# Performance work log

Measured on AMD Instinct MI355X. Metric: run time of the kernel, lower is better.

The kernel has to match this reference:

```python
import jax, jax.numpy as jnp
import numpy as np

N = 100000   # nodes
E = 1000000  # edges (before self-loops)
D = 64       # input_dim
H = 64       # hidden_dim
OUT = 8      # output_dim
G = 128      # num graphs in batch


def setup_inputs() -> dict:
    key = jax.random.key(0)
    ks = jax.random.split(key, 8)
    x = jax.random.normal(ks[0], (N, D), jnp.float32)
    edge_index = jax.random.randint(ks[1], (2, E), 0, N)
    edge_attr = jax.random.uniform(ks[2], (E,), jnp.float32)
    batch = jnp.sort(jax.random.randint(ks[3], (N,), 0, G))
    W1 = jax.random.normal(ks[4], (H, D), jnp.float32) / np.float32(np.sqrt(D))
    b1 = jnp.zeros((H,), jnp.float32)
    W2 = jax.random.normal(ks[5], (OUT, H), jnp.float32) / np.float32(np.sqrt(H))
    b2 = jnp.zeros((OUT,), jnp.float32)
    Wopt = jax.random.normal(ks[6], (1, H), jnp.float32) / np.float32(np.sqrt(H))
    bopt = jnp.zeros((1,), jnp.float32)
    return dict(x=x, edge_index=edge_index, edge_attr=edge_attr, batch=batch,
                W1=W1, b1=b1, W2=W2, b2=b2, Wopt=Wopt, bopt=bopt,
                num_graphs=G)


def gcn_conv(x, edge_index, edge_attr, W, b):
    n = x.shape[0]
    loop = jnp.arange(n)
    # add_self_loops with fill_value=1.0
    row = jnp.concatenate([edge_index[0], loop])
    col = jnp.concatenate([edge_index[1], loop])
    ea = jnp.concatenate([edge_attr, jnp.ones((n,), x.dtype)])
    # degree over row (source); >=1 because of self-loops
    deg = jax.ops.segment_sum(jnp.ones(row.shape, x.dtype), row, num_segments=n)
    dis = deg ** -0.5
    norm = dis[row] * dis[col]
    # message: edge_attr * x_j * norm, gathered from source row
    msg = (ea * norm)[:, None] * x[row]          # [E+N, D]
    aggr = jax.ops.segment_sum(msg, col, num_segments=n)  # scatter-add at target
    return aggr @ W.T + b                        # update: linear


def reference(x, edge_index, edge_attr, batch, W1, b1, W2, b2, Wopt, bopt, num_graphs):
    h = jnp.tanh(gcn_conv(x, edge_index, edge_attr, W1, b1))
    out = jax.nn.sigmoid(h @ W2.T + b2)          # [N, OUT]
    counts = jax.ops.segment_sum(jnp.ones((h.shape[0],), h.dtype), batch,
                                 num_segments=num_graphs)
    gemb = jax.ops.segment_sum(h, batch, num_segments=num_graphs)
    gemb = gemb / jnp.maximum(counts, 1.0)[:, None]  # global_mean_pool
    optimal = jax.nn.sigmoid(gemb @ Wopt.T + bopt)   # [G, 1]
    return (out, optimal)
```

## Files before the change

### kernel.cpp

```cpp
#include <hip/hip_runtime.h>
#include <math.h>
#include <stdint.h>

#define DD 64
#define HH 64
#define OUTD 8
#define NG 128
#define PSPLIT 8
#define NB 512
#define CAPD 3072
#define BIN_CHUNK 4096

typedef short short8 __attribute__((ext_vector_type(8)));
typedef float f32x4 __attribute__((ext_vector_type(4)));

__device__ __forceinline__ float sigmoidf_(float v) { return 1.0f / (1.0f + __expf(-v)); }
__device__ __forceinline__ unsigned short f2bf(float f) {
    unsigned u = __float_as_uint(f);
    unsigned r = u + 0x7FFFu + ((u >> 16) & 1u);
    return (unsigned short)(r >> 16);
}
__device__ __forceinline__ float bf2f(unsigned short b) {
    return __uint_as_float(((unsigned)b) << 16);
}
__device__ __forceinline__ float bflo(unsigned q) { return __uint_as_float(q << 16); }
__device__ __forceinline__ float bfhi(unsigned q) { return __uint_as_float(q & 0xFFFF0000u); }

__global__ void init_kernel(int* gcur, int* scur, float* gemb,
                            const int* __restrict__ batch, int* __restrict__ starts, int N) {
    int t = threadIdx.x;
    for (int i = t; i < NB; i += 256) { gcur[i] = 0; scur[i] = 0; }
    for (int i = t; i < NG * HH; i += 256) gemb[i] = 0.0f;
    if (t <= NG) {
        int g = t, lo = 0, hi = N;
        while (lo < hi) {
            int mid = (lo + hi) >> 1;
            if (batch[mid] < g) lo = mid + 1; else hi = mid;
        }
        starts[g] = lo;
    }
}

__global__ __launch_bounds__(256)
void bin_xcvt_kernel(const int* __restrict__ ei, const float* __restrict__ ea,
                     int* gcur, int* scur, int2* __restrict__ dreg,
                     unsigned char* __restrict__ sreg, int E, int range, int nbin,
                     const float4* __restrict__ x4, uint4* __restrict__ xbf, int n8) {
    if (blockIdx.x >= nbin) {
        int i = (blockIdx.x - nbin) * 256 + threadIdx.x;
        if (i < n8) {
            float4 a = x4[i * 2], b = x4[i * 2 + 1];
            uint4 o;
            o.x = (unsigned)f2bf(a.x) | ((unsigned)f2bf(a.y) << 16);
            o.y = (unsigned)f2bf(a.z) | ((unsigned)f2bf(a.w) << 16);
            o.z = (unsigned)f2bf(b.x) | ((unsigned)f2bf(b.y) << 16);
            o.w = (unsigned)f2bf(b.z) | ((unsigned)f2bf(b.w) << 16);
            xbf[i] = o;
        }
        return;
    }
    __shared__ int dcnt[NB], scnt[NB], dbase[NB], sbase[NB];
    int t = threadIdx.x;
    for (int j = t; j < NB; j += 256) { dcnt[j] = 0; scnt[j] = 0; }
    __syncthreads();
    int e0 = blockIdx.x * BIN_CHUNK;
    int lim = min(BIN_CHUNK, E - e0);
    for (int i = t; i < lim; i += 256) {
        int e = e0 + i;
        atomicAdd(&dcnt[ei[E + e] / range], 1);
        atomicAdd(&scnt[ei[e] / range], 1);
    }
    __syncthreads();
    for (int j = t; j < NB; j += 256) {
        int dc = dcnt[j], sc = scnt[j];
        dbase[j] = dc ? atomicAdd(&gcur[j], dc) : 0;
        sbase[j] = sc ? atomicAdd(&scur[j], sc) : 0;
        dcnt[j] = 0; scnt[j] = 0;
    }
    __syncthreads();
    for (int i = t; i < lim; i += 256) {
        int e = e0 + i;
        int c = ei[E + e];
        int r = ei[e];
        int b = c / range, cl = c - b * range;
        int pos = dbase[b] + atomicAdd(&dcnt[b], 1);
        if (pos < CAPD)
            dreg[(size_t)b * CAPD + pos] = make_int2(r | (cl << 20), __float_as_int(ea[e]));
        int sb = r / range;
        int sp = sbase[sb] + atomicAdd(&scnt[sb], 1);
        if (sp < CAPD)
            sreg[(size_t)sb * CAPD + sp] = (unsigned char)(r - sb * range);
    }
}

__global__ __launch_bounds__(256)
void deg_kernel(const unsigned char* __restrict__ sreg, const int* __restrict__ scur,
                float* __restrict__ dis, int N, int range) {
    __shared__ int cnt[257];
    int t = threadIdx.x, b = blockIdx.x;
    for (int j = t; j <= range; j += 256) cnt[j] = 0;
    __syncthreads();
    int n = min(scur[b], CAPD);
    const unsigned char* p = sreg + (size_t)b * CAPD;
    for (int i = t; i < n; i += 256) atomicAdd(&cnt[p[i]], 1);
    __syncthreads();
    for (int j = t; j < range; j += 256) {
        int node = b * range + j;
        if (node < N) dis[node] = rsqrtf(1.0f + (float)cnt[j]);
    }
}

__global__ __launch_bounds__(256)
void csr_kernel(int2* __restrict__ dreg, const int* __restrict__ gcur,
                const float* __restrict__ dis,
                int* __restrict__ colstart, int* __restrict__ colcnt,
                int N, int range) {
    __shared__ int2 recs[CAPD];
    __shared__ int cnt[257], offs_s[257], sc[256];
    int t = threadIdx.x, b = blockIdx.x;
    int n = min(gcur[b], CAPD);
    size_t base = (size_t)b * CAPD;
    for (int i = t; i < n; i += 256) recs[i] = dreg[base + i];
    for (int j = t; j <= range; j += 256) cnt[j] = 0;
    __syncthreads();
    for (int i = t; i < n; i += 256) atomicAdd(&cnt[recs[i].x >> 20], 1);
    __syncthreads();
    int my = (t < range) ? cnt[t] : 0;
    sc[t] = my;
    __syncthreads();
    for (int off = 1; off < 256; off <<= 1) {
        int v = (t >= off) ? sc[t - off] : 0;
        __syncthreads();
        sc[t] += v;
        __syncthreads();
    }
    int ex = sc[t] - my;
    if (t < range) {
        offs_s[t] = ex;
        int node = b * range + t;
        if (node < N) { colstart[node] = (int)(base + ex); colcnt[node] = my; }
    }
    for (int j = t; j <= range; j += 256) cnt[j] = 0;
    __syncthreads();
    for (int i = t; i < n; i += 256) {
        int2 rc = recs[i];
        int cl = rc.x >> 20;
        int r = rc.x & 0xFFFFF;
        float coef = __int_as_float(rc.y) * dis[r] * dis[b * range + cl];
        int pos = offs_s[cl] + atomicAdd(&cnt[cl], 1);
        dreg[base + pos] = make_int2(r, __float_as_int(coef));
    }
}

__global__ __launch_bounds__(256)
void gather_kernel(const int2* __restrict__ recs,
                   const int* __restrict__ colstart, const int* __restrict__ colcnt,
                   const float* __restrict__ dis,
                   const unsigned short* __restrict__ xbf,
                   unsigned* __restrict__ axb, int N) {
    int wid = blockIdx.x * 4 + (threadIdx.x >> 6);
    int l = threadIdx.x & 63;
    int half = l >> 5, d2 = l & 31;
    int node = wid * 2 + half;
    bool v = node < N;
    float s = v ? dis[node] : 0.f;
    unsigned xv = v ? *(const unsigned*)(xbf + (size_t)node * DD + 2 * d2) : 0u;
    float a0 = s * s * bflo(xv);
    float a1 = s * s * bfhi(xv);
    float b0 = 0.f, b1 = 0.f;
    int cnt = v ? colcnt[node] : 0;
    const int2* p = recs + (v ? colstart[node] : 0);
    int k = 0;
    for (; k + 4 <= cnt; k += 4) {
        int2 r0 = p[k], r1 = p[k + 1], r2 = p[k + 2], r3 = p[k + 3];
        unsigned q0 = *(const unsigned*)(xbf + (size_t)r0.x * DD + 2 * d2);
        unsigned q1 = *(const unsigned*)(xbf + (size_t)r1.x * DD + 2 * d2);
        unsigned q2 = *(const unsigned*)(xbf + (size_t)r2.x * DD + 2 * d2);
        unsigned q3 = *(const unsigned*)(xbf + (size_t)r3.x * DD + 2 * d2);
        float c0 = __int_as_float(r0.y), c1 = __int_as_float(r1.y);
        float c2 = __int_as_float(r2.y), c3 = __int_as_float(r3.y);
        a0 += c0 * bflo(q0); a1 += c0 * bfhi(q0);
        b0 += c1 * bflo(q1); b1 += c1 * bfhi(q1);
        a0 += c2 * bflo(q2); a1 += c2 * bfhi(q2);
        b0 += c3 * bflo(q3); b1 += c3 * bfhi(q3);
    }
    for (; k < cnt; ++k) {
        int2 r0 = p[k];
        unsigned q0 = *(const unsigned*)(xbf + (size_t)r0.x * DD + 2 * d2);
        float c0 = __int_as_float(r0.y);
        a0 += c0 * bflo(q0); a1 += c0 * bfhi(q0);
    }
    if (v) {
        float v0 = a0 + b0, v1 = a1 + b1;
        axb[(size_t)node * (DD / 2) + d2] = (unsigned)f2bf(v0) | ((unsigned)f2bf(v1) << 16);
    }
}

__global__ __launch_bounds__(256)
void head_kernel(const unsigned short* __restrict__ axb,
                 const float* __restrict__ W1, const float* __restrict__ b1,
                 const float* __restrict__ W2, const float* __restrict__ b2,
                 unsigned short* __restrict__ hb, float* __restrict__ outp, int N) {
    __shared__ __align__(16) float htile[4][16][68];
    int tid = threadIdx.x;
    int l = tid & 63, w = tid >> 6;
    int col = l & 15, kg = l >> 4;
    int half = l >> 5, d2 = l & 31;

    short8 w1f[4][2];
    #pragma unroll
    for (int ct = 0; ct < 4; ++ct)
        #pragma unroll
        for (int kt = 0; kt < 2; ++kt) {
            const float* src = W1 + (16 * ct + col) * DD + 32 * kt + 8 * kg;
            short8 f;
            #pragma unroll
            for (int j = 0; j < 8; ++j) f[j] = (short)f2bf(src[j]);
            w1f[ct][kt] = f;
        }
    short8 w2f[2];
    #pragma unroll
    for (int kt = 0; kt < 2; ++kt) {
        short8 f;
        #pragma unroll
        for (int j = 0; j < 8; ++j)
            f[j] = (col < OUTD) ? (short)f2bf(W2[col * HH + 32 * kt + 8 * kg + j]) : (short)0;
        w2f[kt] = f;
    }
    float b1v[4];
    #pragma unroll
    for (int ct = 0; ct < 4; ++ct) b1v[ct] = b1[16 * ct + col];
    float b2v = (col < OUTD) ? b2[col] : 0.f;

    int ngrp = (N + 15) >> 4;
    int g = blockIdx.x * 4 + w;
    bool act = g < ngrp;
    int base = act ? g * 16 : 0;
    int rr = min(base + col, N - 1);

    short8 af[2];
    #pragma unroll
    for (int kt = 0; kt < 2; ++kt)
        af[kt] = *(const short8*)(axb + (size_t)rr * DD + 32 * kt + 8 * kg);

    #pragma unroll
    for (int ct = 0; ct < 4; ++ct) {
        f32x4 acc = {0.f, 0.f, 0.f, 0.f};
        acc = __builtin_amdgcn_mfma_f32_16x16x32_bf16(af[0], w1f[ct][0], acc, 0, 0, 0);
        acc = __builtin_amdgcn_mfma_f32_16x16x32_bf16(af[1], w1f[ct][1], acc, 0, 0, 0);
        #pragma unroll
        for (int jr = 0; jr < 4; ++jr) {
            float v = acc[jr] + b1v[ct];
            float ez = __expf(2.f * v);
            htile[w][4 * kg + jr][16 * ct + col] = (ez - 1.f) / (ez + 1.f);
        }
    }
    __syncthreads();

    #pragma unroll
    for (int it = 0; it < 8; ++it) {
        int node = base + 2 * it + half;
        if (act && node < N) {
            float h0 = htile[w][2 * it + half][2 * d2];
            float h1 = htile[w][2 * it + half][2 * d2 + 1];
            *(unsigned*)(hb + (size_t)node * HH + 2 * d2) =
                (unsigned)f2bf(h0) | ((unsigned)f2bf(h1) << 16);
        }
    }

    short8 hf[2];
    #pragma unroll
    for (int kt = 0; kt < 2; ++kt) {
        const float* src = &htile[w][col][32 * kt + 8 * kg];
        float4 lo = *(const float4*)src;
        float4 hi = *(const float4*)(src + 4);
        short8 f;
        f[0] = (short)f2bf(lo.x); f[1] = (short)f2bf(lo.y);
        f[2] = (short)f2bf(lo.z); f[3] = (short)f2bf(lo.w);
        f[4] = (short)f2bf(hi.x); f[5] = (short)f2bf(hi.y);
        f[6] = (short)f2bf(hi.z); f[7] = (short)f2bf(hi.w);
        hf[kt] = f;
    }
    f32x4 acc2 = {0.f, 0.f, 0.f, 0.f};
    acc2 = __builtin_amdgcn_mfma_f32_16x16x32_bf16(hf[0], w2f[0], acc2, 0, 0, 0);
    acc2 = __builtin_amdgcn_mfma_f32_16x16x32_bf16(hf[1], w2f[1], acc2, 0, 0, 0);
    if (act && col < OUTD) {
        #pragma unroll
        for (int jr = 0; jr < 4; ++jr) {
            int node = base + 4 * kg + jr;
            if (node < N) outp[(size_t)node * OUTD + col] = sigmoidf_(acc2[jr] + b2v);
        }
    }
}

__global__ void pool_kernel(const unsigned short* __restrict__ hb,
                            const int* __restrict__ starts,
                            float* __restrict__ gemb) {
    int g = blockIdx.x / PSPLIT;
    int part = blockIdx.x % PSPLIT;
    int s = starts[g], e = starts[g + 1];
    int tid = threadIdx.x;
    int hc = tid & 63, nl = tid >> 6;
    float sum = 0.0f;
    for (int n = s + part * 4 + nl; n < e; n += PSPLIT * 4)
        sum += bf2f(hb[(size_t)n * HH + hc]);
    __shared__ float red[4][HH];
    red[nl][hc] = sum;
    __syncthreads();
    if (nl == 0) {
        float v = red[0][hc] + red[1][hc] + red[2][hc] + red[3][hc];
        atomicAdd(&gemb[g * HH + hc], v);
    }
}

__global__ void optimal_kernel(const float* __restrict__ gemb,
                               const int* __restrict__ starts,
                               const float* __restrict__ Wopt,
                               const float* __restrict__ bopt,
                               float* __restrict__ out2) {
    int g = blockIdx.x;
    int d = threadIdx.x;
    float c = fmaxf((float)(starts[g + 1] - starts[g]), 1.0f);
    float v = gemb[g * HH + d] / c * Wopt[d];
    #pragma unroll
    for (int off = 32; off > 0; off >>= 1) v += __shfl_down(v, off);
    if (d == 0) out2[g] = 1.0f / (1.0f + __expf(-(v + bopt[0])));
}

extern "C" void kernel_launch(void* const* d_in, const int* in_sizes, int n_in,
                              void* d_out, int out_size, void* d_ws, size_t ws_size,
                              hipStream_t stream) {
    const float* x     = (const float*)d_in[0];
    const int*   ei    = (const int*)d_in[1];
    const float* ea    = (const float*)d_in[2];
    const int*   batch = (const int*)d_in[3];
    const float* W1    = (const float*)d_in[4];
    const float* b1    = (const float*)d_in[5];
    const float* W2    = (const float*)d_in[6];
    const float* b2    = (const float*)d_in[7];
    const float* Wopt  = (const float*)d_in[8];
    const float* bopt  = (const float*)d_in[9];

    int N = in_sizes[0] / DD;
    int E = in_sizes[2];
    int range = (N + NB - 1) / NB;

    float* out  = (float*)d_out;
    float* out2 = out + (size_t)N * OUTD;

    char* p = (char*)d_ws;
    float* dis      = (float*)p;  p += (size_t)N * 4;
    int*   colstart = (int*)p;    p += (size_t)N * 4;
    int*   colcnt   = (int*)p;    p += (size_t)N * 4;
    float* gemb     = (float*)p;  p += (size_t)NG * HH * 4;
    int*   starts   = (int*)p;    p += (size_t)(NG + 2) * 4;
    int*   gcur     = (int*)p;    p += (size_t)NB * 4;
    int*   scur     = (int*)p;    p += (size_t)NB * 4;
    uintptr_t up = (uintptr_t)p; up = (up + 15) & ~(uintptr_t)15; p = (char*)up;
    int2* dreg = (int2*)p;        p += (size_t)NB * CAPD * 8;
    unsigned char* sreg = (unsigned char*)p; p += (size_t)NB * CAPD;
    up = (uintptr_t)p; up = (up + 15) & ~(uintptr_t)15; p = (char*)up;
    unsigned short* xbf = (unsigned short*)p; p += (size_t)N * DD * 2;
    unsigned* axb = (unsigned*)p; p += (size_t)N * (DD / 2) * 4;
    unsigned short* hb  = (unsigned short*)p;

    int n8 = N * DD / 8;
    int nbin = (E + BIN_CHUNK - 1) / BIN_CHUNK;
    int nxc = (n8 + 255) / 256;

    init_kernel<<<1, 256, 0, stream>>>(gcur, scur, gemb, batch, starts, N);
    bin_xcvt_kernel<<<nbin + nxc, 256, 0, stream>>>(ei, ea, gcur, scur, dreg, sreg,
                                                    E, range, nbin,
                                                    (const float4*)x, (uint4*)xbf, n8);
    deg_kernel<<<NB, 256, 0, stream>>>(sreg, scur, dis, N, range);
    csr_kernel<<<NB, 256, 0, stream>>>(dreg, gcur, dis, colstart, colcnt, N, range);

    gather_kernel<<<(N + 7) / 8, 256, 0, stream>>>(dreg, colstart, colcnt, dis, xbf, axb, N);

    int ngrp = (N + 15) / 16;
    head_kernel<<<(ngrp + 3) / 4, 256, 0, stream>>>((const unsigned short*)axb,
                                                    W1, b1, W2, b2, hb, out, N);

    pool_kernel<<<NG * PSPLIT, 256, 0, stream>>>(hb, starts, gemb);
    optimal_kernel<<<NG, 64, 0, stream>>>(gemb, starts, Wopt, bopt, out2);
}
```

Baseline: 147.4 us.

## Cache edges in registers during binning, use shift-based bins, drop init kernel

The binning kernel now runs with 1024 threads. Each thread loads its four edges (row, col, attr) into registers once, so the count and scatter passes no longer re-read edge_index. Bins are now a fixed 256 nodes, selected with shifts and masks instead of integer division, so there are about 391 bins instead of 512 and each bin holds more edges within the same CAPD capacity. The init kernel is replaced by two hipMemsetAsync calls, and pool/optimal recompute graph starts by binary search over batch instead of reading a precomputed array. This assumes scur sits directly after gcur so a single memset clears both, and it narrows the headroom before bin overflow.

```diff
diff --git a/kernel.cpp b/kernel.cpp
--- a/kernel.cpp
+++ b/kernel.cpp
@@ -8,8 +8,11 @@
 #define NG 128
 #define PSPLIT 8
 #define NB 512
+#define RSH 8
+#define RMSK 255
 #define CAPD 3072
 #define BIN_CHUNK 4096
+#define BT 1024
 
 typedef short short8 __attribute__((ext_vector_type(8)));
 typedef float f32x4 __attribute__((ext_vector_type(4)));
@@ -26,28 +29,19 @@
 __device__ __forceinline__ float bflo(unsigned q) { return __uint_as_float(q << 16); }
 __device__ __forceinline__ float bfhi(unsigned q) { return __uint_as_float(q & 0xFFFF0000u); }
 
-__global__ void init_kernel(int* gcur, int* scur, float* gemb,
-                            const int* __restrict__ batch, int* __restrict__ starts, int N) {
-    int t = threadIdx.x;
-    for (int i = t; i < NB; i += 256) { gcur[i] = 0; scur[i] = 0; }
-    for (int i = t; i < NG * HH; i += 256) gemb[i] = 0.0f;
-    if (t <= NG) {
-        int g = t, lo = 0, hi = N;
-        while (lo < hi) {
-            int mid = (lo + hi) >> 1;
-            if (batch[mid] < g) lo = mid + 1; else hi = mid;
-        }
-        starts[g] = lo;
-    }
-}
-
-__global__ __launch_bounds__(256)
+__device__ __forceinline__ int lbound_(const int* __restrict__ batch, int N, int g) {
+    int lo = 0, hi = N;
+    while (lo < hi) { int m = (lo + hi) >> 1; if (batch[m] < g) lo = m + 1; else hi = m; }
+    return lo;
+}
+
+__global__ __launch_bounds__(BT)
 void bin_xcvt_kernel(const int* __restrict__ ei, const float* __restrict__ ea,
                      int* gcur, int* scur, int2* __restrict__ dreg,
-                     unsigned char* __restrict__ sreg, int E, int range, int nbin,
+                     unsigned char* __restrict__ sreg, int E, int nbin,
                      const float4* __restrict__ x4, uint4* __restrict__ xbf, int n8) {
     if (blockIdx.x >= nbin) {
-        int i = (blockIdx.x - nbin) * 256 + threadIdx.x;
+        int i = (blockIdx.x - nbin) * BT + threadIdx.x;
         if (i < n8) {
             float4 a = x4[i * 2], b = x4[i * 2 + 1];
             uint4 o;
@@ -61,71 +55,78 @@
     }
     __shared__ int dcnt[NB], scnt[NB], dbase[NB], sbase[NB];
     int t = threadIdx.x;
-    for (int j = t; j < NB; j += 256) { dcnt[j] = 0; scnt[j] = 0; }
+    for (int j = t; j < NB; j += BT) { dcnt[j] = 0; scnt[j] = 0; }
     __syncthreads();
     int e0 = blockIdx.x * BIN_CHUNK;
     int lim = min(BIN_CHUNK, E - e0);
-    for (int i = t; i < lim; i += 256) {
-        int e = e0 + i;
-        atomicAdd(&dcnt[ei[E + e] / range], 1);
-        atomicAdd(&scnt[ei[e] / range], 1);
-    }
-    __syncthreads();
-    for (int j = t; j < NB; j += 256) {
+    int rv0 = 0, rv1 = 0, rv2 = 0, rv3 = 0;
+    int cv0 = 0, cv1 = 0, cv2 = 0, cv3 = 0;
+    float av0 = 0, av1 = 0, av2 = 0, av3 = 0;
+    {
+        int i;
+        i = t;            if (i < lim) { rv0 = ei[e0+i]; cv0 = ei[E+e0+i]; av0 = ea[e0+i];
+                                         atomicAdd(&dcnt[cv0 >> RSH], 1); atomicAdd(&scnt[rv0 >> RSH], 1); }
+        i = t + BT;       if (i < lim) { rv1 = ei[e0+i]; cv1 = ei[E+e0+i]; av1 = ea[e0+i];
+                                         atomicAdd(&dcnt[cv1 >> RSH], 1); atomicAdd(&scnt[rv1 >> RSH], 1); }
+        i = t + 2 * BT;   if (i < lim) { rv2 = ei[e0+i]; cv2 = ei[E+e0+i]; av2 = ea[e0+i];
+                                         atomicAdd(&dcnt[cv2 >> RSH], 1); atomicAdd(&scnt[rv2 >> RSH], 1); }
+        i = t + 3 * BT;   if (i < lim) { rv3 = ei[e0+i]; cv3 = ei[E+e0+i]; av3 = ea[e0+i];
+                                         atomicAdd(&dcnt[cv3 >> RSH], 1); atomicAdd(&scnt[rv3 >> RSH], 1); }
+    }
+    __syncthreads();
+    for (int j = t; j < NB; j += BT) {
         int dc = dcnt[j], sc = scnt[j];
         dbase[j] = dc ? atomicAdd(&gcur[j], dc) : 0;
         sbase[j] = sc ? atomicAdd(&scur[j], sc) : 0;
         dcnt[j] = 0; scnt[j] = 0;
     }
     __syncthreads();
-    for (int i = t; i < lim; i += 256) {
-        int e = e0 + i;
-        int c = ei[E + e];
-        int r = ei[e];
-        int b = c / range, cl = c - b * range;
-        int pos = dbase[b] + atomicAdd(&dcnt[b], 1);
-        if (pos < CAPD)
-            dreg[(size_t)b * CAPD + pos] = make_int2(r | (cl << 20), __float_as_int(ea[e]));
-        int sb = r / range;
-        int sp = sbase[sb] + atomicAdd(&scnt[sb], 1);
-        if (sp < CAPD)
-            sreg[(size_t)sb * CAPD + sp] = (unsigned char)(r - sb * range);
-    }
+    #define EMIT(RR, CC, AA, II) do { \
+        if ((II) < lim) { \
+            int b_ = (CC) >> RSH, cl_ = (CC) & RMSK; \
+            int pos_ = dbase[b_] + atomicAdd(&dcnt[b_], 1); \
+            if (pos_ < CAPD) dreg[(size_t)b_ * CAPD + pos_] = make_int2((RR) | (cl_ << 20), __float_as_int(AA)); \
+            int sb_ = (RR) >> RSH; \
+            int sp_ = sbase[sb_] + atomicAdd(&scnt[sb_], 1); \
+            if (sp_ < CAPD) sreg[(size_t)sb_ * CAPD + sp_] = (unsigned char)((RR) & RMSK); \
+        } } while (0)
+    EMIT(rv0, cv0, av0, t);
+    EMIT(rv1, cv1, av1, t + BT);
+    EMIT(rv2, cv2, av2, t + 2 * BT);
+    EMIT(rv3, cv3, av3, t + 3 * BT);
+    #undef EMIT
 }
 
 __global__ __launch_bounds__(256)
 void deg_kernel(const unsigned char* __restrict__ sreg, const int* __restrict__ scur,
-                float* __restrict__ dis, int N, int range) {
-    __shared__ int cnt[257];
+                float* __restrict__ dis, int N) {
+    __shared__ int cnt[256];
     int t = threadIdx.x, b = blockIdx.x;
-    for (int j = t; j <= range; j += 256) cnt[j] = 0;
+    cnt[t] = 0;
     __syncthreads();
     int n = min(scur[b], CAPD);
     const unsigned char* p = sreg + (size_t)b * CAPD;
     for (int i = t; i < n; i += 256) atomicAdd(&cnt[p[i]], 1);
     __syncthreads();
-    for (int j = t; j < range; j += 256) {
-        int node = b * range + j;
-        if (node < N) dis[node] = rsqrtf(1.0f + (float)cnt[j]);
-    }
+    int node = (b << RSH) + t;
+    if (node < N) dis[node] = rsqrtf(1.0f + (float)cnt[t]);
 }
 
 __global__ __launch_bounds__(256)
 void csr_kernel(int2* __restrict__ dreg, const int* __restrict__ gcur,
                 const float* __restrict__ dis,
-                int* __restrict__ colstart, int* __restrict__ colcnt,
-                int N, int range) {
+                int* __restrict__ colstart, int* __restrict__ colcnt, int N) {
     __shared__ int2 recs[CAPD];
-    __shared__ int cnt[257], offs_s[257], sc[256];
+    __shared__ int cnt[256], offs_s[256], sc[256];
     int t = threadIdx.x, b = blockIdx.x;
     int n = min(gcur[b], CAPD);
     size_t base = (size_t)b * CAPD;
     for (int i = t; i < n; i += 256) recs[i] = dreg[base + i];
-    for (int j = t; j <= range; j += 256) cnt[j] = 0;
+    cnt[t] = 0;
     __syncthreads();
     for (int i = t; i < n; i += 256) atomicAdd(&cnt[recs[i].x >> 20], 1);
     __syncthreads();
-    int my = (t < range) ? cnt[t] : 0;
+    int my = cnt[t];
     sc[t] = my;
     __syncthreads();
     for (int off = 1; off < 256; off <<= 1) {
@@ -135,18 +136,16 @@
         __syncthreads();
     }
     int ex = sc[t] - my;
-    if (t < range) {
-        offs_s[t] = ex;
-        int node = b * range + t;
-        if (node < N) { colstart[node] = (int)(base + ex); colcnt[node] = my; }
-    }
-    for (int j = t; j <= range; j += 256) cnt[j] = 0;
+    offs_s[t] = ex;
+    int node = (b << RSH) + t;
+    if (node < N) { colstart[node] = (int)(base + ex); colcnt[node] = my; }
+    cnt[t] = 0;
     __syncthreads();
     for (int i = t; i < n; i += 256) {
         int2 rc = recs[i];
         int cl = rc.x >> 20;
         int r = rc.x & 0xFFFFF;
-        float coef = __int_as_float(rc.y) * dis[r] * dis[b * range + cl];
+        float coef = __int_as_float(rc.y) * dis[r] * dis[(b << RSH) + cl];
         int pos = offs_s[cl] + atomicAdd(&cnt[cl], 1);
         dreg[base + pos] = make_int2(r, __float_as_int(coef));
     }
@@ -294,11 +293,12 @@
 }
 
 __global__ void pool_kernel(const unsigned short* __restrict__ hb,
-                            const int* __restrict__ starts,
+                            const int* __restrict__ batch, int N,
                             float* __restrict__ gemb) {
     int g = blockIdx.x / PSPLIT;
     int part = blockIdx.x % PSPLIT;
-    int s = starts[g], e = starts[g + 1];
+    int s = lbound_(batch, N, g);
+    int e = lbound_(batch, N, g + 1);
     int tid = threadIdx.x;
     int hc = tid & 63, nl = tid >> 6;
     float sum = 0.0f;
@@ -314,13 +314,15 @@
 }
 
 __global__ void optimal_kernel(const float* __restrict__ gemb,
-                               const int* __restrict__ starts,
+                               const int* __restrict__ batch, int N,
                                const float* __restrict__ Wopt,
                                const float* __restrict__ bopt,
                                float* __restrict__ out2) {
     int g = blockIdx.x;
     int d = threadIdx.x;
-    float c = fmaxf((float)(starts[g + 1] - starts[g]), 1.0f);
+    int s = lbound_(batch, N, g);
+    int e = lbound_(batch, N, g + 1);
+    float c = fmaxf((float)(e - s), 1.0f);
     float v = gemb[g * HH + d] / c * Wopt[d];
     #pragma unroll
     for (int off = 32; off > 0; off >>= 1) v += __shfl_down(v, off);
@@ -343,7 +345,7 @@
 
     int N = in_sizes[0] / DD;
     int E = in_sizes[2];
-    int range = (N + NB - 1) / NB;
+    int nbins = (N + 255) >> 8;
 
     float* out  = (float*)d_out;
     float* out2 = out + (size_t)N * OUTD;
@@ -353,12 +355,11 @@
     int*   colstart = (int*)p;    p += (size_t)N * 4;
     int*   colcnt   = (int*)p;    p += (size_t)N * 4;
     float* gemb     = (float*)p;  p += (size_t)NG * HH * 4;
-    int*   starts   = (int*)p;    p += (size_t)(NG + 2) * 4;
     int*   gcur     = (int*)p;    p += (size_t)NB * 4;
     int*   scur     = (int*)p;    p += (size_t)NB * 4;
     uintptr_t up = (uintptr_t)p; up = (up + 15) & ~(uintptr_t)15; p = (char*)up;
-    int2* dreg = (int2*)p;        p += (size_t)NB * CAPD * 8;
-    unsigned char* sreg = (unsigned char*)p; p += (size_t)NB * CAPD;
+    int2* dreg = (int2*)p;        p += (size_t)nbins * CAPD * 8;
+    unsigned char* sreg = (unsigned char*)p; p += (size_t)nbins * CAPD;
     up = (uintptr_t)p; up = (up + 15) & ~(uintptr_t)15; p = (char*)up;
     unsigned short* xbf = (unsigned short*)p; p += (size_t)N * DD * 2;
     unsigned* axb = (unsigned*)p; p += (size_t)N * (DD / 2) * 4;
@@ -366,14 +367,16 @@
 
     int n8 = N * DD / 8;
     int nbin = (E + BIN_CHUNK - 1) / BIN_CHUNK;
-    int nxc = (n8 + 255) / 256;
-
-    init_kernel<<<1, 256, 0, stream>>>(gcur, scur, gemb, batch, starts, N);
-    bin_xcvt_kernel<<<nbin + nxc, 256, 0, stream>>>(ei, ea, gcur, scur, dreg, sreg,
-                                                    E, range, nbin,
-                                                    (const float4*)x, (uint4*)xbf, n8);
-    deg_kernel<<<NB, 256, 0, stream>>>(sreg, scur, dis, N, range);
-    csr_kernel<<<NB, 256, 0, stream>>>(dreg, gcur, dis, colstart, colcnt, N, range);
+    int nxc = (n8 + BT - 1) / BT;
+
+    hipMemsetAsync(gcur, 0, (size_t)NB * 8, stream);
+    hipMemsetAsync(gemb, 0, (size_t)NG * HH * 4, stream);
+
+    bin_xcvt_kernel<<<nbin + nxc, BT, 0, stream>>>(ei, ea, gcur, scur, dreg, sreg,
+                                                   E, nbin,
+                                                   (const float4*)x, (uint4*)xbf, n8);
+    deg_kernel<<<nbins, 256, 0, stream>>>(sreg, scur, dis, N);
+    csr_kernel<<<nbins, 256, 0, stream>>>(dreg, gcur, dis, colstart, colcnt, N);
 
     gather_kernel<<<(N + 7) / 8, 256, 0, stream>>>(dreg, colstart, colcnt, dis, xbf, axb, N);
 
@@ -381,6 +384,6 @@
     head_kernel<<<(ngrp + 3) / 4, 256, 0, stream>>>((const unsigned short*)axb,
                                                     W1, b1, W2, b2, hb, out, N);
 
-    pool_kernel<<<NG * PSPLIT, 256, 0, stream>>>(hb, starts, gemb);
-    optimal_kernel<<<NG, 64, 0, stream>>>(gemb, starts, Wopt, bopt, out2);
-}
+    pool_kernel<<<NG * PSPLIT, 256, 0, stream>>>(hb, batch, N, gemb);
+    optimal_kernel<<<NG, 64, 0, stream>>>(gemb, batch, N, Wopt, bopt, out2);
+}
```

New measurement: 133.6 us. 1.1x faster.
